# Performance work log

Hardware: AMD Instinct MI355X
Metric: run time of the kernel (lower is better)

Reference implementation:

```python
import jax, jax.numpy as jnp
import numpy as np

SQRT_QKV_DIM = 8.0  # sqrt(qkv_dim=64)


def setup_inputs() -> dict:
    key = jax.random.key(0)
    ks = jax.random.split(key, 8)
    B, H, T, M, d, hid = 4, 16, 512, 512, 64, 16
    return {
        "q": jax.random.normal(ks[0], (B, H, T, d), dtype=jnp.float32),
        "k": jax.random.normal(ks[1], (B, H, M, d), dtype=jnp.float32),
        "v": jax.random.normal(ks[2], (B, H, M, d), dtype=jnp.float32),
        "D_TM": jax.random.uniform(ks[3], (B, T, M), dtype=jnp.float32),
        "mix1_weight": jax.random.uniform(ks[4], (H, 2, hid), minval=-0.7071, maxval=0.7071, dtype=jnp.float32),
        "mix1_bias": jax.random.uniform(ks[5], (H, hid), minval=-0.7071, maxval=0.7071, dtype=jnp.float32),
        "mix2_weight": jax.random.uniform(ks[6], (H, hid, 1), minval=-0.25, maxval=0.25, dtype=jnp.float32),
        "mix2_bias": jax.random.uniform(ks[7], (H, 1), minval=-0.25, maxval=0.25, dtype=jnp.float32),
    }


def reference(q, k, v, D_TM, mix1_weight, mix1_bias, mix2_weight, mix2_bias):
    B, H, T, d = q.shape
    Mc = k.shape[2]
    # scaled dot-product score: (B,H,T,M)
    dot_score = jnp.einsum("bhtd,bhmd->bhtm", q, k) / SQRT_QKV_DIM
    # per-head 2->hidden->1 MLP mixing dot score and distance bias.
    # Avoid explicit stack: linear layer over the 2 score channels expands as
    # dot*W1[:,0,:] + D*W1[:,1,:].  ms1: (B,H,T,M,hid)
    w1_dot = mix1_weight[:, 0, :][None, :, None, None, :]   # (1,H,1,1,hid)
    w1_dist = mix1_weight[:, 1, :][None, :, None, None, :]
    ms1 = (dot_score[..., None] * w1_dot
           + D_TM[:, None, :, :, None] * w1_dist
           + mix1_bias[None, :, None, None, :])
    ms1 = jax.nn.relu(ms1)
    # hidden -> 1: mixed_scores (B,H,T,M)
    mixed = jnp.einsum("bhtmc,hc->bhtm", ms1, mix2_weight[:, :, 0])
    mixed = mixed + mix2_bias[:, 0][None, :, None, None]
    weights = jax.nn.softmax(mixed, axis=3)
    out = jnp.einsum("bhtm,bhmd->bhtd", weights, v)   # (B,H,T,d)
    return out.transpose(0, 2, 1, 3).reshape(B, T, H * d)
```

## Files before the change

### kernel.cpp

```cpp
#include <hip/hip_runtime.h>
#include <stdint.h>

typedef __attribute__((ext_vector_type(8))) short short8;
typedef __attribute__((ext_vector_type(4))) float floatx4;

#define MFMA(a, b, c) __builtin_amdgcn_mfma_f32_16x16x32_bf16(a, b, c, 0, 0, 0)

union Frag { uint32_t u[4]; short8 s; };

__device__ __forceinline__ void packsplit(float a, float b, uint32_t& hi, uint32_t& lo) {
    uint32_t ua = __float_as_uint(a), ub = __float_as_uint(b);
    uint32_t ha = ua & 0xFFFF0000u, hb = ub & 0xFFFF0000u;
    float ra = a - __uint_as_float(ha);
    float rb = b - __uint_as_float(hb);
    hi = (ha >> 16) | hb;
    lo = (__float_as_uint(ra) >> 16) | (__float_as_uint(rb) & 0xFFFF0000u);
}

__device__ __forceinline__ float fexp2(float x) {
#if __has_builtin(__builtin_amdgcn_exp2f)
    return __builtin_amdgcn_exp2f(x);
#else
    return exp2f(x);
#endif
}


__global__ __launch_bounds__(512, 4)
void msmha_flash(const float* __restrict__ qg, const float* __restrict__ kg,
                 const float* __restrict__ vg, const float* __restrict__ Dg,
                 const float* __restrict__ m1w, const float* __restrict__ m1b,
                 const float* __restrict__ m2w, const float* __restrict__ m2b,
                 float* __restrict__ outg) {
    __shared__ __align__(16) uint32_t sm[18432];
    __shared__ __align__(16) float4 wlds[16];

    const int tid   = threadIdx.x;
    const int w     = tid >> 6;
    const int group = w >> 2;
    const int gw    = w & 3;
    const int lane  = tid & 63;
    const int col   = lane & 15;
    const int quad  = lane >> 4;
    const int gtid  = tid & 255;

    const int bid = blockIdx.x;
    const int wgT = bid & 7;
    const int bh  = bid >> 3;
    const int h   = bh & 15;
    const int b   = bh >> 4;
    const int t0g = wgT * 64;

    const size_t base = (size_t)bh * 512 * 64;
    const float LOG2E = 1.4426950408889634f;

    if (tid < 16) {
        const float w1d = m1w[h * 32 + tid];
        const float w1s = m1w[h * 32 + 16 + tid];
        const float b1  = m1b[h * 16 + tid];
        const float w2  = m2w[h * 16 + tid];
        wlds[tid] = make_float4(w1d * (0.125f * LOG2E), w1s * LOG2E, b1 * LOG2E, 0.5f * w2);
    }

    float sA = 0.f, sB = 0.f, sC = 0.f;
#pragma unroll 1
    for (int c = 0; c < 16; ++c) {
        const float w2 = m2w[h * 16 + c];
        sA = fmaf(w2, m1w[h * 32 + c], sA);
        sB = fmaf(w2, m1w[h * 32 + 16 + c], sB);
        sC = fmaf(w2, m1b[h * 16 + c], sC);
    }
    const float Ac = sA * (0.0625f * LOG2E);
    const float Bc = sB * (0.5f * LOG2E);
    const float Cc = fmaf(0.5f, sC, m2b[h]) * LOG2E;

    Frag qh[2], ql[2];
    {
        const float* qrow = qg + base + (size_t)(t0g + gw * 16 + col) * 64;
#pragma unroll
        for (int ks = 0; ks < 2; ++ks) {
            const float4 f0 = *(const float4*)(qrow + ks * 32 + quad * 8);
            const float4 f1 = *(const float4*)(qrow + ks * 32 + quad * 8 + 4);
            packsplit(f0.x, f0.y, qh[ks].u[0], ql[ks].u[0]);
            packsplit(f0.z, f0.w, qh[ks].u[1], ql[ks].u[1]);
            packsplit(f1.x, f1.y, qh[ks].u[2], ql[ks].u[2]);
            packsplit(f1.z, f1.w, qh[ks].u[3], ql[ks].u[3]);
        }
    }

    const int ml0  = gtid >> 4;
    const int k4   = gtid & 15;
    const int dgrp = gtid & 15;
    const int m4   = gtid >> 4;
    const int cpV  = (2 * m4 + 8 * ((dgrp >> 1) & 3)) & 31;
    const int rsel = col >> 3;

    const int gb = group * 9216;
    uint32_t* KH = sm + gb;
    uint32_t* KL = sm + gb + 2304;
    uint32_t* VH = sm + gb + 4608;
    uint32_t* VL = sm + gb + 6912;

    const int moff = group * 256;
    const float* kc = kg + base + (size_t)moff * 64;
    const float* vc = vg + base + (size_t)moff * 64;
    const float* Dc = Dg + ((size_t)b * 512 + t0g + gw * 16 + col) * 512 + moff + quad * 4;

    float run_m = -3.0e38f, run_l = 0.f;
    floatx4 oacc[4];
#pragma unroll
    for (int dt = 0; dt < 4; ++dt) oacc[dt] = floatx4{0.f, 0.f, 0.f, 0.f};

#pragma unroll 1
    for (int mc = 0; mc < 4; ++mc) {
        const float* kp = kc + (size_t)mc * 64 * 64;
        const float* vp = vc + (size_t)mc * 64 * 64;

        float4 kr[4], vr[4];
#pragma unroll
        for (int it = 0; it < 4; ++it)
            kr[it] = *(const float4*)(kp + (size_t)(ml0 + it * 16) * 64 + k4 * 4);
#pragma unroll
        for (int i = 0; i < 4; ++i)
            vr[i] = *(const float4*)(vp + (size_t)(4 * m4 + i) * 64 + dgrp * 4);
        float dvf[16];
#pragma unroll
        for (int mt = 0; mt < 4; ++mt) {
            const float4 dd = *(const float4*)(Dc + mc * 64 + mt * 16);
            dvf[mt * 4 + 0] = dd.x; dvf[mt * 4 + 1] = dd.y;
            dvf[mt * 4 + 2] = dd.z; dvf[mt * 4 + 3] = dd.w;
        }

#pragma unroll
        for (int it = 0; it < 4; ++it) {
            uint32_t h0, l0, h1, l1;
            packsplit(kr[it].x, kr[it].y, h0, l0);
            packsplit(kr[it].z, kr[it].w, h1, l1);
            const int ml = ml0 + it * 16;
            *(uint2*)(KH + ml * 36 + 2 * k4) = make_uint2(h0, h1);
            *(uint2*)(KL + ml * 36 + 2 * k4) = make_uint2(l0, l1);
        }
        __syncthreads();

        floatx4 sc[4];
#pragma unroll
        for (int mt = 0; mt < 4; ++mt) {
            floatx4 acc = {0.f, 0.f, 0.f, 0.f};
#pragma unroll
            for (int ks = 0; ks < 2; ++ks) {
                const int ro = (mt * 16 + col) * 36 + 16 * ks + 4 * quad;
                Frag ah, al;
                ah.s = *(const short8*)(KH + ro);
                al.s = *(const short8*)(KL + ro);
                acc = MFMA(ah.s, qh[ks].s, acc);
                acc = MFMA(ah.s, ql[ks].s, acc);
                acc = MFMA(al.s, qh[ks].s, acc);
            }
            sc[mt] = acc;
        }

        float mix[16];
#pragma unroll
        for (int e = 0; e < 16; ++e) mix[e] = fmaf(dvf[e], Bc, Cc);
#pragma unroll 4
        for (int c = 0; c < 16; ++c) {
            const float4 wv = wlds[c];
#pragma unroll
            for (int mt = 0; mt < 4; ++mt)
#pragma unroll
                for (int r = 0; r < 4; ++r) {
                    const float hh = fmaf(sc[mt][r], wv.x, fmaf(dvf[mt * 4 + r], wv.y, wv.z));
                    mix[mt * 4 + r] = fmaf(fabsf(hh), wv.w, mix[mt * 4 + r]);
                }
        }
#pragma unroll
        for (int mt = 0; mt < 4; ++mt)
#pragma unroll
            for (int r = 0; r < 4; ++r)
                sc[mt][r] = fmaf(sc[mt][r], Ac, mix[mt * 4 + r]);

#pragma unroll
        for (int jj = 0; jj < 4; ++jj) {
            uint32_t h0, l0, h1, l1;
            packsplit(((const float*)&vr[0])[jj], ((const float*)&vr[1])[jj], h0, l0);
            packsplit(((const float*)&vr[2])[jj], ((const float*)&vr[3])[jj], h1, l1);
            const int d = 4 * dgrp + jj;
            *(uint2*)(VH + d * 36 + cpV) = make_uint2(h0, h1);
            *(uint2*)(VL + d * 36 + cpV) = make_uint2(l0, l1);
        }

        float cmx = -3.0e38f;
#pragma unroll
        for (int mt = 0; mt < 4; ++mt)
#pragma unroll
            for (int r = 0; r < 4; ++r) cmx = fmaxf(cmx, sc[mt][r]);
        cmx = fmaxf(cmx, __shfl_xor(cmx, 16, 64));
        cmx = fmaxf(cmx, __shfl_xor(cmx, 32, 64));
        const float nm    = fmaxf(run_m, cmx);
        const float scale = fexp2(run_m - nm);
        float csum = 0.f;
#pragma unroll
        for (int mt = 0; mt < 4; ++mt)
#pragma unroll
            for (int r = 0; r < 4; ++r) {
                const float p = fexp2(sc[mt][r] - nm);
                sc[mt][r] = p;
                csum += p;
            }
        csum += __shfl_xor(csum, 16, 64);
        csum += __shfl_xor(csum, 32, 64);
        run_l = fmaf(run_l, scale, csum);
        run_m = nm;
        float sOT[4];
#pragma unroll
        for (int r = 0; r < 4; ++r) sOT[r] = __shfl(scale, quad * 4 + r, 64);
#pragma unroll
        for (int dt = 0; dt < 4; ++dt)
#pragma unroll
            for (int r = 0; r < 4; ++r) oacc[dt][r] *= sOT[r];

        __syncthreads();

        const int prow = (gw * 16 + col) * 36;
#pragma unroll
        for (int mt = 0; mt < 4; ++mt) {
            uint32_t h0, l0, h1, l1;
            packsplit(sc[mt][0], sc[mt][1], h0, l0);
            packsplit(sc[mt][2], sc[mt][3], h1, l1);
            *(uint2*)(KH + prow + mt * 8 + 2 * quad) = make_uint2(h0, h1);
            *(uint2*)(KL + prow + mt * 8 + 2 * quad) = make_uint2(l0, l1);
        }

#pragma unroll
        for (int ks = 0; ks < 2; ++ks) {
            const int po = prow + 16 * ks + 4 * quad;
            Frag pah, pal;
            pah.s = *(const short8*)(KH + po);
            pal.s = *(const short8*)(KL + po);
#pragma unroll
            for (int dt = 0; dt < 4; ++dt) {
                const int cbd = ((16 * ks + 4 * quad) + 8 * ((2 * dt + rsel) & 3)) & 31;
                const int vo = (dt * 16 + col) * 36 + cbd;
                Frag bhv, blv;
                bhv.s = *(const short8*)(VH + vo);
                blv.s = *(const short8*)(VL + vo);
                oacc[dt] = MFMA(pah.s, bhv.s, oacc[dt]);
                oacc[dt] = MFMA(pah.s, blv.s, oacc[dt]);
                oacc[dt] = MFMA(pal.s, bhv.s, oacc[dt]);
            }
        }
        __syncthreads();
    }

    float* smf = (float*)sm;
    if (group == 1) {
        if (quad == 0) {
            smf[13376 + gw * 16 + col] = run_m;
            smf[13440 + gw * 16 + col] = run_l;
        }
        const int t = gw * 16 + quad * 4;
#pragma unroll
        for (int dt = 0; dt < 4; ++dt)
#pragma unroll
            for (int r = 0; r < 4; ++r)
                smf[9216 + (t + r) * 65 + dt * 16 + col] = oacc[dt][r];
    }
    __syncthreads();
    if (group == 0) {
        const float m1c = smf[13376 + gw * 16 + col];
        const float l1c = smf[13440 + gw * 16 + col];
        const float M   = fmaxf(run_m, m1c);
        const float s0  = fexp2(run_m - M);
        const float s1  = fexp2(m1c - M);
        const float rdn = 1.f / fmaf(run_l, s0, l1c * s1);
        float s0T[4], s1T[4], rdT[4];
#pragma unroll
        for (int r = 0; r < 4; ++r) {
            s0T[r] = __shfl(s0, quad * 4 + r, 64);
            s1T[r] = __shfl(s1, quad * 4 + r, 64);
            rdT[r] = __shfl(rdn, quad * 4 + r, 64);
        }
        const int t = gw * 16 + quad * 4;
        const size_t obase = ((size_t)b * 512 + t0g + t) * 1024 + h * 64 + col;
#pragma unroll
        for (int dt = 0; dt < 4; ++dt)
#pragma unroll
            for (int r = 0; r < 4; ++r) {
                const float o1 = smf[9216 + (t + r) * 65 + dt * 16 + col];
                outg[obase + (size_t)r * 1024 + dt * 16] =
                    fmaf(oacc[dt][r], s0T[r], o1 * s1T[r]) * rdT[r];
            }
    }
}

extern "C" void kernel_launch(void* const* d_in, const int* in_sizes, int n_in,
                              void* d_out, int out_size, void* d_ws, size_t ws_size,
                              hipStream_t stream) {
    const float* q   = (const float*)d_in[0];
    const float* k   = (const float*)d_in[1];
    const float* v   = (const float*)d_in[2];
    const float* dtm = (const float*)d_in[3];
    const float* m1w = (const float*)d_in[4];
    const float* m1b = (const float*)d_in[5];
    const float* m2w = (const float*)d_in[6];
    const float* m2b = (const float*)d_in[7];
    float* out = (float*)d_out;

    dim3 grid(4 * 16 * 8);
    dim3 block(512);
    msmha_flash<<<grid, block, 0, stream>>>(q, k, v, dtm, m1w, m1b, m2w, m2b, out);
}
```

Baseline: 132.4 us.

## Prefetch next K/V/D chunk into registers and lighten barriers

Double-buffers the global loads of K, V and the distance tile in registers so the next chunk's loads are issued while the current chunk is being computed, and fully unrolls the chunk loop. It replaces __syncthreads with a barrier that waits only on LDS counters (lgkmcnt) so that in-flight global prefetches are not drained at each barrier. It also raises wave priority around the MFMA sections and uses v_perm for the bf16 split packing. The cost is higher register pressure from the doubled buffers under launch_bounds(512,4), which may cause spills or lower occupancy.

After: 139.5 us. 5.3% more time.

```diff
diff --git a/kernel.cpp b/kernel.cpp
--- a/kernel.cpp
+++ b/kernel.cpp
@@ -13,8 +13,8 @@
     uint32_t ha = ua & 0xFFFF0000u, hb = ub & 0xFFFF0000u;
     float ra = a - __uint_as_float(ha);
     float rb = b - __uint_as_float(hb);
-    hi = (ha >> 16) | hb;
-    lo = (__float_as_uint(ra) >> 16) | (__float_as_uint(rb) & 0xFFFF0000u);
+    hi = __builtin_amdgcn_perm(ub, ua, 0x07060302u);
+    lo = __builtin_amdgcn_perm(__float_as_uint(rb), __float_as_uint(ra), 0x07060302u);
 }
 
 __device__ __forceinline__ float fexp2(float x) {
@@ -23,6 +23,12 @@
 #else
     return exp2f(x);
 #endif
+}
+
+__device__ __forceinline__ void bar_lds() {
+    asm volatile("s_waitcnt lgkmcnt(0)" ::: "memory");
+    __builtin_amdgcn_s_barrier();
+    __builtin_amdgcn_sched_barrier(0);
 }
 
 
@@ -62,6 +68,35 @@
         wlds[tid] = make_float4(w1d * (0.125f * LOG2E), w1s * LOG2E, b1 * LOG2E, 0.5f * w2);
     }
 
+    const int ml0  = gtid >> 4;
+    const int k4   = gtid & 15;
+    const int dgrp = gtid & 15;
+    const int m4   = gtid >> 4;
+    const int cpV  = (2 * m4 + 8 * ((dgrp >> 1) & 3)) & 31;
+    const int rsel = col >> 3;
+
+    const int gb = group * 9216;
+    uint32_t* KH = sm + gb;
+    uint32_t* KL = sm + gb + 2304;
+    uint32_t* VH = sm + gb + 4608;
+    uint32_t* VL = sm + gb + 6912;
+
+    const int moff = group * 256;
+    const float* kc = kg + base + (size_t)moff * 64;
+    const float* vc = vg + base + (size_t)moff * 64;
+    const float* Dc = Dg + ((size_t)b * 512 + t0g + gw * 16 + col) * 512 + moff + quad * 4;
+
+    float4 kp[2][4], vp[2][4], dp[2][4];
+#pragma unroll
+    for (int it = 0; it < 4; ++it)
+        kp[0][it] = *(const float4*)(kc + (size_t)(ml0 + it * 16) * 64 + k4 * 4);
+#pragma unroll
+    for (int mt = 0; mt < 4; ++mt)
+        dp[0][mt] = *(const float4*)(Dc + mt * 16);
+#pragma unroll
+    for (int i = 0; i < 4; ++i)
+        vp[0][i] = *(const float4*)(vc + (size_t)(4 * m4 + i) * 64 + dgrp * 4);
+
     float sA = 0.f, sB = 0.f, sC = 0.f;
 #pragma unroll 1
     for (int c = 0; c < 16; ++c) {
@@ -88,61 +123,34 @@
         }
     }
 
-    const int ml0  = gtid >> 4;
-    const int k4   = gtid & 15;
-    const int dgrp = gtid & 15;
-    const int m4   = gtid >> 4;
-    const int cpV  = (2 * m4 + 8 * ((dgrp >> 1) & 3)) & 31;
-    const int rsel = col >> 3;
-
-    const int gb = group * 9216;
-    uint32_t* KH = sm + gb;
-    uint32_t* KL = sm + gb + 2304;
-    uint32_t* VH = sm + gb + 4608;
-    uint32_t* VL = sm + gb + 6912;
-
-    const int moff = group * 256;
-    const float* kc = kg + base + (size_t)moff * 64;
-    const float* vc = vg + base + (size_t)moff * 64;
-    const float* Dc = Dg + ((size_t)b * 512 + t0g + gw * 16 + col) * 512 + moff + quad * 4;
-
     float run_m = -3.0e38f, run_l = 0.f;
     floatx4 oacc[4];
 #pragma unroll
     for (int dt = 0; dt < 4; ++dt) oacc[dt] = floatx4{0.f, 0.f, 0.f, 0.f};
 
-#pragma unroll 1
+#pragma unroll
     for (int mc = 0; mc < 4; ++mc) {
-        const float* kp = kc + (size_t)mc * 64 * 64;
-        const float* vp = vc + (size_t)mc * 64 * 64;
-
-        float4 kr[4], vr[4];
-#pragma unroll
-        for (int it = 0; it < 4; ++it)
-            kr[it] = *(const float4*)(kp + (size_t)(ml0 + it * 16) * 64 + k4 * 4);
-#pragma unroll
-        for (int i = 0; i < 4; ++i)
-            vr[i] = *(const float4*)(vp + (size_t)(4 * m4 + i) * 64 + dgrp * 4);
-        float dvf[16];
-#pragma unroll
-        for (int mt = 0; mt < 4; ++mt) {
-            const float4 dd = *(const float4*)(Dc + mc * 64 + mt * 16);
-            dvf[mt * 4 + 0] = dd.x; dvf[mt * 4 + 1] = dd.y;
-            dvf[mt * 4 + 2] = dd.z; dvf[mt * 4 + 3] = dd.w;
-        }
+        const int cur = mc & 1, nxt = cur ^ 1;
 
 #pragma unroll
         for (int it = 0; it < 4; ++it) {
             uint32_t h0, l0, h1, l1;
-            packsplit(kr[it].x, kr[it].y, h0, l0);
-            packsplit(kr[it].z, kr[it].w, h1, l1);
+            packsplit(kp[cur][it].x, kp[cur][it].y, h0, l0);
+            packsplit(kp[cur][it].z, kp[cur][it].w, h1, l1);
             const int ml = ml0 + it * 16;
             *(uint2*)(KH + ml * 36 + 2 * k4) = make_uint2(h0, h1);
             *(uint2*)(KL + ml * 36 + 2 * k4) = make_uint2(l0, l1);
         }
-        __syncthreads();
+        if (mc < 3) {
+            const float* kn = kc + (size_t)(mc + 1) * 64 * 64;
+#pragma unroll
+            for (int it = 0; it < 4; ++it)
+                kp[nxt][it] = *(const float4*)(kn + (size_t)(ml0 + it * 16) * 64 + k4 * 4);
+        }
+        bar_lds();
 
         floatx4 sc[4];
+        __builtin_amdgcn_s_setprio(1);
 #pragma unroll
         for (int mt = 0; mt < 4; ++mt) {
             floatx4 acc = {0.f, 0.f, 0.f, 0.f};
@@ -158,7 +166,14 @@
             }
             sc[mt] = acc;
         }
-
+        __builtin_amdgcn_s_setprio(0);
+
+        float dvf[16];
+#pragma unroll
+        for (int mt = 0; mt < 4; ++mt) {
+            dvf[mt * 4 + 0] = dp[cur][mt].x; dvf[mt * 4 + 1] = dp[cur][mt].y;
+            dvf[mt * 4 + 2] = dp[cur][mt].z; dvf[mt * 4 + 3] = dp[cur][mt].w;
+        }
         float mix[16];
 #pragma unroll
         for (int e = 0; e < 16; ++e) mix[e] = fmaf(dvf[e], Bc, Cc);
@@ -179,14 +194,26 @@
             for (int r = 0; r < 4; ++r)
                 sc[mt][r] = fmaf(sc[mt][r], Ac, mix[mt * 4 + r]);
 
+        if (mc < 3) {
+#pragma unroll
+            for (int mt = 0; mt < 4; ++mt)
+                dp[nxt][mt] = *(const float4*)(Dc + (mc + 1) * 64 + mt * 16);
+        }
+
 #pragma unroll
         for (int jj = 0; jj < 4; ++jj) {
             uint32_t h0, l0, h1, l1;
-            packsplit(((const float*)&vr[0])[jj], ((const float*)&vr[1])[jj], h0, l0);
-            packsplit(((const float*)&vr[2])[jj], ((const float*)&vr[3])[jj], h1, l1);
+            packsplit(((const float*)&vp[cur][0])[jj], ((const float*)&vp[cur][1])[jj], h0, l0);
+            packsplit(((const float*)&vp[cur][2])[jj], ((const float*)&vp[cur][3])[jj], h1, l1);
             const int d = 4 * dgrp + jj;
             *(uint2*)(VH + d * 36 + cpV) = make_uint2(h0, h1);
             *(uint2*)(VL + d * 36 + cpV) = make_uint2(l0, l1);
+        }
+        if (mc < 3) {
+            const float* vn = vc + (size_t)(mc + 1) * 64 * 64;
+#pragma unroll
+            for (int i = 0; i < 4; ++i)
+                vp[nxt][i] = *(const float4*)(vn + (size_t)(4 * m4 + i) * 64 + dgrp * 4);
         }
 
         float cmx = -3.0e38f;
@@ -219,7 +246,7 @@
 #pragma unroll
             for (int r = 0; r < 4; ++r) oacc[dt][r] *= sOT[r];
 
-        __syncthreads();
+        bar_lds();
 
         const int prow = (gw * 16 + col) * 36;
 #pragma unroll
@@ -231,6 +258,7 @@
             *(uint2*)(KL + prow + mt * 8 + 2 * quad) = make_uint2(l0, l1);
         }
 
+        __builtin_amdgcn_s_setprio(1);
 #pragma unroll
         for (int ks = 0; ks < 2; ++ks) {
             const int po = prow + 16 * ks + 4 * quad;
@@ -249,14 +277,17 @@
                 oacc[dt] = MFMA(pal.s, bhv.s, oacc[dt]);
             }
         }
-        __syncthreads();
-    }
-
+        __builtin_amdgcn_s_setprio(0);
+
+        bar_lds();
+    }
+
+    const float rv_part = run_l;
     float* smf = (float*)sm;
     if (group == 1) {
         if (quad == 0) {
             smf[13376 + gw * 16 + col] = run_m;
-            smf[13440 + gw * 16 + col] = run_l;
+            smf[13440 + gw * 16 + col] = rv_part;
         }
         const int t = gw * 16 + quad * 4;
 #pragma unroll
@@ -265,7 +296,7 @@
             for (int r = 0; r < 4; ++r)
                 smf[9216 + (t + r) * 65 + dt * 16 + col] = oacc[dt][r];
     }
-    __syncthreads();
+    bar_lds();
     if (group == 0) {
         const float m1c = smf[13376 + gw * 16 + col];
         const float l1c = smf[13440 + gw * 16 + col];
```
